# Kernel tuning notes

Hardware: AMD Instinct MI355X
Metric: run time of the kernel (lower is better)

Reference implementation:

```python
import jax, jax.numpy as jnp
import numpy as np

NUM_USERS = 100000
NUM_ITEMS = 50000
NUM_EDGES = 1000000
HIDDEN = 128


def setup_inputs() -> dict:
    key = jax.random.key(0)
    ks = jax.random.split(key, 8)
    z_user = jax.random.normal(ks[0], (NUM_USERS, HIDDEN), dtype=jnp.float32)
    z_item = jax.random.normal(ks[1], (NUM_ITEMS, HIDDEN), dtype=jnp.float32)
    row_idx = jax.random.randint(ks[2], (NUM_EDGES,), 0, NUM_USERS, dtype=jnp.int64 if jax.config.jax_enable_x64 else jnp.int32)
    col_idx = jax.random.randint(ks[3], (NUM_EDGES,), 0, NUM_ITEMS, dtype=jnp.int64 if jax.config.jax_enable_x64 else jnp.int32)
    # Linear params (PyTorch Linear: y = x @ W.T + b); store as [in, out] for einsum.
    scale1 = 1.0 / np.sqrt(2 * HIDDEN)
    scale2 = 1.0 / np.sqrt(HIDDEN)
    W1 = jax.random.uniform(ks[4], (2 * HIDDEN, HIDDEN), jnp.float32, -scale1, scale1)
    b1 = jax.random.uniform(ks[5], (HIDDEN,), jnp.float32, -scale1, scale1)
    W2 = jax.random.uniform(ks[6], (HIDDEN, 1), jnp.float32, -scale2, scale2)
    b2 = jax.random.uniform(ks[7], (1,), jnp.float32, -scale2, scale2)
    return {"z_user": z_user, "z_item": z_item, "row_idx": row_idx,
            "col_idx": col_idx, "W1": W1, "b1": b1, "W2": W2, "b2": b2}


def reference(z_user, z_item, row_idx, col_idx, W1, b1, W2, b2):
    # Gather endpoint embeddings for each candidate edge: [E, H] each.
    zu = z_user[row_idx]
    zi = z_item[col_idx]
    # Equivalent to concat([zu, zi]) @ W1 without materializing the concat:
    h = zu @ W1[:HIDDEN] + zi @ W1[HIDDEN:] + b1  # [E, H]
    h = jax.nn.relu(h)
    out = h @ W2 + b2  # [E, 1]
    return out
```

## Files before the change

kernel.cpp:

```cpp
#include <hip/hip_runtime.h>
#include <hip/hip_bf16.h>
#include <stdint.h>

#define H 128
#define NU 100000
#define NI 50000

typedef __attribute__((ext_vector_type(8))) short short8;
typedef __attribute__((ext_vector_type(4))) float f32x4;

__device__ __forceinline__ uint16_t f2bf(float f) {
    uint32_t x = __float_as_uint(f);
    return (uint16_t)((x + 0x7fffu + ((x >> 16) & 1u)) >> 16);
}
__device__ __forceinline__ uint32_t cvtpk(float lo, float hi) {
    uint32_t r;
    asm("v_cvt_pk_bf16_f32 %0, %1, %2" : "=v"(r) : "v"(lo), "v"(hi));
    return r;
}
__device__ __forceinline__ float cvt_ub0(uint32_t v) { float f; asm("v_cvt_f32_ubyte0 %0, %1" : "=v"(f) : "v"(v)); return f; }
__device__ __forceinline__ float cvt_ub1(uint32_t v) { float f; asm("v_cvt_f32_ubyte1 %0, %1" : "=v"(f) : "v"(v)); return f; }
__device__ __forceinline__ float cvt_ub2(uint32_t v) { float f; asm("v_cvt_f32_ubyte2 %0, %1" : "=v"(f) : "v"(v)); return f; }
__device__ __forceinline__ float cvt_ub3(uint32_t v) { float f; asm("v_cvt_f32_ubyte3 %0, %1" : "=v"(f) : "v"(v)); return f; }

__device__ __forceinline__ int lds_off(int row, int k) {
    return (row * 256 + k * 2) ^ ((row & 7) << 4);
}


__global__ __launch_bounds__(256) void wconv_kernel(
    const float* __restrict__ W1, uint16_t* __restrict__ Wt)
{
    __shared__ char lds[32768];
    const int half = blockIdx.x;
    const float* W = W1 + (size_t)half * H * H;
    uint16_t* Out = Wt + (size_t)half * H * H;
    const int tid = threadIdx.x;

    int n4 = (tid & 31) * 4;
    int k  = tid >> 5;
    #pragma unroll
    for (int p = 0; p < 16; ++p, k += 8) {
        f32x4 v = *(const f32x4*)(W + (size_t)k * H + n4);
        *(uint16_t*)(lds + lds_off(n4 + 0, k)) = f2bf(v.x);
        *(uint16_t*)(lds + lds_off(n4 + 1, k)) = f2bf(v.y);
        *(uint16_t*)(lds + lds_off(n4 + 2, k)) = f2bf(v.z);
        *(uint16_t*)(lds + lds_off(n4 + 3, k)) = f2bf(v.w);
    }
    __syncthreads();
    int n = tid >> 1;
    #pragma unroll
    for (int p = 0; p < 8; ++p) {
        int chunk = (tid & 1) * 8 + p;
        uint4 v = *(const uint4*)(lds + lds_off(n, chunk * 8));
        *(uint4*)(Out + (size_t)n * H + chunk * 8) = v;
    }
}

__global__ __launch_bounds__(256) void proj_kernel(
    const float* __restrict__ z_user, const float* __restrict__ z_item,
    const uint16_t* __restrict__ Wt, const float* __restrict__ b1,
    uint8_t* __restrict__ U8, uint8_t* __restrict__ I8,
    float* __restrict__ Us, float* __restrict__ Is, int nub)
{
    __shared__ char lds[32768];

    int bid = blockIdx.x;
    const float* Z; const uint16_t* Wth; uint8_t* Out8; float* Sc; int M; bool addb1;
    if (bid < nub) { Z = z_user; Wth = Wt;         Out8 = U8; Sc = Us; M = NU; addb1 = false; }
    else { bid -= nub; Z = z_item; Wth = Wt + H*H; Out8 = I8; Sc = Is; M = NI; addb1 = true; }
    const int row0 = bid * 128;
    const int tid = threadIdx.x;

    {
        int n = tid >> 1;
        #pragma unroll
        for (int p = 0; p < 8; ++p) {
            int chunk = (tid & 1) * 8 + p;
            uint4 v = *(const uint4*)(Wth + (size_t)n * H + chunk * 8);
            *(uint4*)(lds + lds_off(n, chunk * 8)) = v;
        }
    }
    __syncthreads();

    const int w  = tid >> 6;
    const int l  = tid & 63;
    const int lr = l & 15;
    const int lk = (l >> 4) * 8;

    int r0 = row0 + w * 32 + lr;
    int r1 = r0 + 16;
    const float* a0p = Z + (size_t)(r0 < M ? r0 : M - 1) * H;
    const float* a1p = Z + (size_t)(r1 < M ? r1 : M - 1) * H;

    f32x4 acc[2][8];
    #pragma unroll
    for (int m0 = 0; m0 < 2; ++m0)
        #pragma unroll
        for (int n0 = 0; n0 < 8; ++n0)
            acc[m0][n0] = (f32x4){0.f, 0.f, 0.f, 0.f};

    #pragma unroll
    for (int kk = 0; kk < 4; ++kk) {
        int kb = kk * 32 + lk;
        f32x4 v00 = *(const f32x4*)(a0p + kb);
        f32x4 v01 = *(const f32x4*)(a0p + kb + 4);
        f32x4 v10 = *(const f32x4*)(a1p + kb);
        f32x4 v11 = *(const f32x4*)(a1p + kb + 4);
        short8 a0, a1;
        uint32_t* A0 = (uint32_t*)&a0;
        uint32_t* A1 = (uint32_t*)&a1;
        A0[0] = cvtpk(v00.x, v00.y); A0[1] = cvtpk(v00.z, v00.w);
        A0[2] = cvtpk(v01.x, v01.y); A0[3] = cvtpk(v01.z, v01.w);
        A1[0] = cvtpk(v10.x, v10.y); A1[1] = cvtpk(v10.z, v10.w);
        A1[2] = cvtpk(v11.x, v11.y); A1[3] = cvtpk(v11.z, v11.w);
        #pragma unroll
        for (int n0 = 0; n0 < 8; ++n0) {
            short8 b = *(const short8*)(lds + lds_off(n0*16 + lr, kb));
            acc[0][n0] = __builtin_amdgcn_mfma_f32_16x16x32_bf16(a0, b, acc[0][n0], 0, 0, 0);
            acc[1][n0] = __builtin_amdgcn_mfma_f32_16x16x32_bf16(a1, b, acc[1][n0], 0, 0, 0);
        }
    }

    float b1v[8];
    #pragma unroll
    for (int n0 = 0; n0 < 8; ++n0) b1v[n0] = addb1 ? b1[n0*16 + lr] : 0.f;

    const int rbase = row0 + w * 32;
    #pragma unroll
    for (int m0 = 0; m0 < 2; ++m0) {
        #pragma unroll
        for (int ri = 0; ri < 4; ++ri) {
            int gr = rbase + m0*16 + (l >> 4) * 4 + ri;
            float v[8];
            float am = 0.f;
            #pragma unroll
            for (int n0 = 0; n0 < 8; ++n0) {
                v[n0] = acc[m0][n0][ri] + b1v[n0];
                am = fmaxf(am, fabsf(v[n0]));
            }
            am = fmaxf(am, __shfl_xor(am, 1));
            am = fmaxf(am, __shfl_xor(am, 2));
            am = fmaxf(am, __shfl_xor(am, 4));
            am = fmaxf(am, __shfl_xor(am, 8));
            float s = am * (1.0f / 127.0f);
            float r = 127.0f / fmaxf(am, 1e-30f);
            uint32_t lo = 0, hi = 0;
            #pragma unroll
            for (int n0 = 0; n0 < 4; ++n0) {
                uint32_t q8 = (uint32_t)fmaf(v[n0], r, 128.5f);
                lo |= q8 << (8 * n0);
            }
            #pragma unroll
            for (int n0 = 4; n0 < 8; ++n0) {
                uint32_t q8 = (uint32_t)fmaf(v[n0], r, 128.5f);
                hi |= q8 << (8 * (n0 - 4));
            }
            if (gr < M) {
                *(uint2*)(Out8 + (size_t)gr * H + lr * 8) = make_uint2(lo, hi);
                if (lr == 0) Sc[gr] = s;
            }
        }
    }
}

__device__ __forceinline__ float edge_dot16(uint4 u, uint4 i, float su, float si,
                                            const float* w2v) {
    const float k = -128.0f * (su + si);
    const uint32_t* up = &u.x;
    const uint32_t* ip = &i.x;
    float acc = 0.f, h;
    #pragma unroll
    for (int d = 0; d < 4; ++d) {
        h = fmaf(su, cvt_ub0(up[d]), fmaf(si, cvt_ub0(ip[d]), k)); acc = fmaf(fmaxf(h, 0.f), w2v[4*d+0], acc);
        h = fmaf(su, cvt_ub1(up[d]), fmaf(si, cvt_ub1(ip[d]), k)); acc = fmaf(fmaxf(h, 0.f), w2v[4*d+1], acc);
        h = fmaf(su, cvt_ub2(up[d]), fmaf(si, cvt_ub2(ip[d]), k)); acc = fmaf(fmaxf(h, 0.f), w2v[4*d+2], acc);
        h = fmaf(su, cvt_ub3(up[d]), fmaf(si, cvt_ub3(ip[d]), k)); acc = fmaf(fmaxf(h, 0.f), w2v[4*d+3], acc);
    }
    return acc;
}

__device__ __forceinline__ float group_reduce8(float acc) {
    acc += __shfl_xor(acc, 4);
    acc += __shfl_xor(acc, 2);
    acc += __shfl_xor(acc, 1);
    return acc;
}

__global__ __launch_bounds__(256) void edge_kernel(
    const uint8_t* __restrict__ U8, const uint8_t* __restrict__ I8,
    const float* __restrict__ Us, const float* __restrict__ Is,
    const int* __restrict__ row_idx, const int* __restrict__ col_idx,
    const float* __restrict__ W2, const float* __restrict__ b2p,
    float* __restrict__ out, int E)
{
    const int l = threadIdx.x & 63;
    const int g = l >> 3;
    const int t = l & 7;

    float w2v[16];
    #pragma unroll
    for (int j = 0; j < 16; ++j) w2v[j] = W2[(j & 7) * 16 + 2 * t + (j >> 3)];
    const float b2 = *b2p;

    const int wid = (int)((blockIdx.x * blockDim.x + threadIdx.x) >> 6);
    const int nw  = (int)((gridDim.x * blockDim.x) >> 6);
    const int stride = nw * 32;
    const int toff = t * 16;

    for (int e0 = wid * 32 + g * 4; e0 + 3 < E; e0 += stride) {
        int4 rp = *(const int4*)(row_idx + e0);
        int4 cp = *(const int4*)(col_idx + e0);
        uint4 u0 = *(const uint4*)(U8 + (uint32_t)(rp.x * H + toff));
        uint4 i0 = *(const uint4*)(I8 + (uint32_t)(cp.x * H + toff));
        uint4 u1 = *(const uint4*)(U8 + (uint32_t)(rp.y * H + toff));
        uint4 i1 = *(const uint4*)(I8 + (uint32_t)(cp.y * H + toff));
        uint4 u2 = *(const uint4*)(U8 + (uint32_t)(rp.z * H + toff));
        uint4 i2 = *(const uint4*)(I8 + (uint32_t)(cp.z * H + toff));
        uint4 u3 = *(const uint4*)(U8 + (uint32_t)(rp.w * H + toff));
        uint4 i3 = *(const uint4*)(I8 + (uint32_t)(cp.w * H + toff));
        float su0 = Us[rp.x], si0 = Is[cp.x];
        float su1 = Us[rp.y], si1 = Is[cp.y];
        float su2 = Us[rp.z], si2 = Is[cp.z];
        float su3 = Us[rp.w], si3 = Is[cp.w];
        float a0 = group_reduce8(edge_dot16(u0, i0, su0, si0, w2v));
        float a1 = group_reduce8(edge_dot16(u1, i1, su1, si1, w2v));
        float a2 = group_reduce8(edge_dot16(u2, i2, su2, si2, w2v));
        float a3 = group_reduce8(edge_dot16(u3, i3, su3, si3, w2v));
        if (t == 0) {
            f32x4 o; o.x = a0 + b2; o.y = a1 + b2; o.z = a2 + b2; o.w = a3 + b2;
            *(f32x4*)(out + e0) = o;
        }
    }
    if (wid == 0 && g == 0) {
        for (int e = (E & ~3); e < E; ++e) {
            int r = row_idx[e], c = col_idx[e];
            uint4 uv = *(const uint4*)(U8 + (uint32_t)(r * H + toff));
            uint4 iv = *(const uint4*)(I8 + (uint32_t)(c * H + toff));
            float acc = group_reduce8(edge_dot16(uv, iv, Us[r], Is[c], w2v));
            if (t == 0) out[e] = acc + b2;
        }
    }
}

extern "C" void kernel_launch(void* const* d_in, const int* in_sizes, int n_in,
                              void* d_out, int out_size, void* d_ws, size_t ws_size,
                              hipStream_t stream) {
    const float* z_user = (const float*)d_in[0];
    const float* z_item = (const float*)d_in[1];
    const int*   row_idx = (const int*)d_in[2];
    const int*   col_idx = (const int*)d_in[3];
    const float* W1 = (const float*)d_in[4];
    const float* b1 = (const float*)d_in[5];
    const float* W2 = (const float*)d_in[6];
    const float* b2 = (const float*)d_in[7];
    float* out = (float*)d_out;
    const int E = in_sizes[2];

    uint8_t* U8 = (uint8_t*)d_ws;
    uint8_t* I8 = U8 + (size_t)NU * H;
    float*   Us = (float*)(I8 + (size_t)NI * H);
    float*   Is = Us + NU;
    uint16_t* Wt = (uint16_t*)(Is + NI);

    const int nub = (NU + 127) / 128;
    const int nib = (NI + 127) / 128;
    wconv_kernel<<<2, 256, 0, stream>>>(W1, Wt);
    proj_kernel<<<nub + nib, 256, 0, stream>>>(z_user, z_item, Wt, b1, U8, I8, Us, Is, nub);
    edge_kernel<<<2048, 256, 0, stream>>>(U8, I8, Us, Is, row_idx, col_idx, W2, b2, out, E);
}
```

Measured before the change: 69.80 us.

## Use 512-thread projection blocks with one M-tile per wave and prefetch edge indices

The projection kernel moves from 256 to 512 threads per block, with each wave handling 16 rows instead of 32. This halves per-thread accumulator registers and doubles waves per block, aiming for better latency hiding on the fp32 embedding loads. The edge kernel now loads the next iteration's row and column indices before gathering the current embeddings, so index-load latency overlaps the dependent gathers. The cost is more waves sharing each LDS copy of the weights, plus extra live registers for the prefetched indices.

```diff
diff --git a/kernel.cpp b/kernel.cpp
--- a/kernel.cpp
+++ b/kernel.cpp
@@ -57,7 +57,7 @@
     }
 }
 
-__global__ __launch_bounds__(256) void proj_kernel(
+__global__ __launch_bounds__(512) void proj_kernel(
     const float* __restrict__ z_user, const float* __restrict__ z_item,
     const uint16_t* __restrict__ Wt, const float* __restrict__ b1,
     uint8_t* __restrict__ U8, uint8_t* __restrict__ I8,
@@ -73,10 +73,10 @@
     const int tid = threadIdx.x;
 
     {
-        int n = tid >> 1;
-        #pragma unroll
-        for (int p = 0; p < 8; ++p) {
-            int chunk = (tid & 1) * 8 + p;
+        int n = tid >> 2;
+        #pragma unroll
+        for (int p = 0; p < 4; ++p) {
+            int chunk = (tid & 3) * 4 + p;
             uint4 v = *(const uint4*)(Wth + (size_t)n * H + chunk * 8);
             *(uint4*)(lds + lds_off(n, chunk * 8)) = v;
         }
@@ -88,37 +88,27 @@
     const int lr = l & 15;
     const int lk = (l >> 4) * 8;
 
-    int r0 = row0 + w * 32 + lr;
-    int r1 = r0 + 16;
+    int r0 = row0 + w * 16 + lr;
     const float* a0p = Z + (size_t)(r0 < M ? r0 : M - 1) * H;
-    const float* a1p = Z + (size_t)(r1 < M ? r1 : M - 1) * H;
-
-    f32x4 acc[2][8];
-    #pragma unroll
-    for (int m0 = 0; m0 < 2; ++m0)
-        #pragma unroll
-        for (int n0 = 0; n0 < 8; ++n0)
-            acc[m0][n0] = (f32x4){0.f, 0.f, 0.f, 0.f};
+
+    f32x4 acc[8];
+    #pragma unroll
+    for (int n0 = 0; n0 < 8; ++n0)
+        acc[n0] = (f32x4){0.f, 0.f, 0.f, 0.f};
 
     #pragma unroll
     for (int kk = 0; kk < 4; ++kk) {
         int kb = kk * 32 + lk;
         f32x4 v00 = *(const f32x4*)(a0p + kb);
         f32x4 v01 = *(const f32x4*)(a0p + kb + 4);
-        f32x4 v10 = *(const f32x4*)(a1p + kb);
-        f32x4 v11 = *(const f32x4*)(a1p + kb + 4);
-        short8 a0, a1;
+        short8 a0;
         uint32_t* A0 = (uint32_t*)&a0;
-        uint32_t* A1 = (uint32_t*)&a1;
         A0[0] = cvtpk(v00.x, v00.y); A0[1] = cvtpk(v00.z, v00.w);
         A0[2] = cvtpk(v01.x, v01.y); A0[3] = cvtpk(v01.z, v01.w);
-        A1[0] = cvtpk(v10.x, v10.y); A1[1] = cvtpk(v10.z, v10.w);
-        A1[2] = cvtpk(v11.x, v11.y); A1[3] = cvtpk(v11.z, v11.w);
         #pragma unroll
         for (int n0 = 0; n0 < 8; ++n0) {
             short8 b = *(const short8*)(lds + lds_off(n0*16 + lr, kb));
-            acc[0][n0] = __builtin_amdgcn_mfma_f32_16x16x32_bf16(a0, b, acc[0][n0], 0, 0, 0);
-            acc[1][n0] = __builtin_amdgcn_mfma_f32_16x16x32_bf16(a1, b, acc[1][n0], 0, 0, 0);
+            acc[n0] = __builtin_amdgcn_mfma_f32_16x16x32_bf16(a0, b, acc[n0], 0, 0, 0);
         }
     }
 
@@ -126,40 +116,37 @@
     #pragma unroll
     for (int n0 = 0; n0 < 8; ++n0) b1v[n0] = addb1 ? b1[n0*16 + lr] : 0.f;
 
-    const int rbase = row0 + w * 32;
-    #pragma unroll
-    for (int m0 = 0; m0 < 2; ++m0) {
-        #pragma unroll
-        for (int ri = 0; ri < 4; ++ri) {
-            int gr = rbase + m0*16 + (l >> 4) * 4 + ri;
-            float v[8];
-            float am = 0.f;
-            #pragma unroll
-            for (int n0 = 0; n0 < 8; ++n0) {
-                v[n0] = acc[m0][n0][ri] + b1v[n0];
-                am = fmaxf(am, fabsf(v[n0]));
-            }
-            am = fmaxf(am, __shfl_xor(am, 1));
-            am = fmaxf(am, __shfl_xor(am, 2));
-            am = fmaxf(am, __shfl_xor(am, 4));
-            am = fmaxf(am, __shfl_xor(am, 8));
-            float s = am * (1.0f / 127.0f);
-            float r = 127.0f / fmaxf(am, 1e-30f);
-            uint32_t lo = 0, hi = 0;
-            #pragma unroll
-            for (int n0 = 0; n0 < 4; ++n0) {
-                uint32_t q8 = (uint32_t)fmaf(v[n0], r, 128.5f);
-                lo |= q8 << (8 * n0);
-            }
-            #pragma unroll
-            for (int n0 = 4; n0 < 8; ++n0) {
-                uint32_t q8 = (uint32_t)fmaf(v[n0], r, 128.5f);
-                hi |= q8 << (8 * (n0 - 4));
-            }
-            if (gr < M) {
-                *(uint2*)(Out8 + (size_t)gr * H + lr * 8) = make_uint2(lo, hi);
-                if (lr == 0) Sc[gr] = s;
-            }
+    const int rbase = row0 + w * 16;
+    #pragma unroll
+    for (int ri = 0; ri < 4; ++ri) {
+        int gr = rbase + (l >> 4) * 4 + ri;
+        float v[8];
+        float am = 0.f;
+        #pragma unroll
+        for (int n0 = 0; n0 < 8; ++n0) {
+            v[n0] = acc[n0][ri] + b1v[n0];
+            am = fmaxf(am, fabsf(v[n0]));
+        }
+        am = fmaxf(am, __shfl_xor(am, 1));
+        am = fmaxf(am, __shfl_xor(am, 2));
+        am = fmaxf(am, __shfl_xor(am, 4));
+        am = fmaxf(am, __shfl_xor(am, 8));
+        float s = am * (1.0f / 127.0f);
+        float r = 127.0f / fmaxf(am, 1e-30f);
+        uint32_t lo = 0, hi = 0;
+        #pragma unroll
+        for (int n0 = 0; n0 < 4; ++n0) {
+            uint32_t q8 = (uint32_t)fmaf(v[n0], r, 128.5f);
+            lo |= q8 << (8 * n0);
+        }
+        #pragma unroll
+        for (int n0 = 4; n0 < 8; ++n0) {
+            uint32_t q8 = (uint32_t)fmaf(v[n0], r, 128.5f);
+            hi |= q8 << (8 * (n0 - 4));
+        }
+        if (gr < M) {
+            *(uint2*)(Out8 + (size_t)gr * H + lr * 8) = make_uint2(lo, hi);
+            if (lr == 0) Sc[gr] = s;
         }
     }
 }
@@ -207,29 +194,39 @@
     const int nw  = (int)((gridDim.x * blockDim.x) >> 6);
     const int stride = nw * 32;
     const int toff = t * 16;
-
-    for (int e0 = wid * 32 + g * 4; e0 + 3 < E; e0 += stride) {
+    const int e0 = wid * 32 + g * 4;
+
+    if (e0 + 3 < E) {
         int4 rp = *(const int4*)(row_idx + e0);
         int4 cp = *(const int4*)(col_idx + e0);
-        uint4 u0 = *(const uint4*)(U8 + (uint32_t)(rp.x * H + toff));
-        uint4 i0 = *(const uint4*)(I8 + (uint32_t)(cp.x * H + toff));
-        uint4 u1 = *(const uint4*)(U8 + (uint32_t)(rp.y * H + toff));
-        uint4 i1 = *(const uint4*)(I8 + (uint32_t)(cp.y * H + toff));
-        uint4 u2 = *(const uint4*)(U8 + (uint32_t)(rp.z * H + toff));
-        uint4 i2 = *(const uint4*)(I8 + (uint32_t)(cp.z * H + toff));
-        uint4 u3 = *(const uint4*)(U8 + (uint32_t)(rp.w * H + toff));
-        uint4 i3 = *(const uint4*)(I8 + (uint32_t)(cp.w * H + toff));
-        float su0 = Us[rp.x], si0 = Is[cp.x];
-        float su1 = Us[rp.y], si1 = Is[cp.y];
-        float su2 = Us[rp.z], si2 = Is[cp.z];
-        float su3 = Us[rp.w], si3 = Is[cp.w];
-        float a0 = group_reduce8(edge_dot16(u0, i0, su0, si0, w2v));
-        float a1 = group_reduce8(edge_dot16(u1, i1, su1, si1, w2v));
-        float a2 = group_reduce8(edge_dot16(u2, i2, su2, si2, w2v));
-        float a3 = group_reduce8(edge_dot16(u3, i3, su3, si3, w2v));
-        if (t == 0) {
-            f32x4 o; o.x = a0 + b2; o.y = a1 + b2; o.z = a2 + b2; o.w = a3 + b2;
-            *(f32x4*)(out + e0) = o;
+        for (int e = e0; e + 3 < E; e += stride) {
+            int en = e + stride;
+            int4 rpn = rp, cpn = cp;
+            if (en + 3 < E) {
+                rpn = *(const int4*)(row_idx + en);
+                cpn = *(const int4*)(col_idx + en);
+            }
+            uint4 u0 = *(const uint4*)(U8 + (uint32_t)(rp.x * H + toff));
+            uint4 i0 = *(const uint4*)(I8 + (uint32_t)(cp.x * H + toff));
+            uint4 u1 = *(const uint4*)(U8 + (uint32_t)(rp.y * H + toff));
+            uint4 i1 = *(const uint4*)(I8 + (uint32_t)(cp.y * H + toff));
+            uint4 u2 = *(const uint4*)(U8 + (uint32_t)(rp.z * H + toff));
+            uint4 i2 = *(const uint4*)(I8 + (uint32_t)(cp.z * H + toff));
+            uint4 u3 = *(const uint4*)(U8 + (uint32_t)(rp.w * H + toff));
+            uint4 i3 = *(const uint4*)(I8 + (uint32_t)(cp.w * H + toff));
+            float su0 = Us[rp.x], si0 = Is[cp.x];
+            float su1 = Us[rp.y], si1 = Is[cp.y];
+            float su2 = Us[rp.z], si2 = Is[cp.z];
+            float su3 = Us[rp.w], si3 = Is[cp.w];
+            float a0 = group_reduce8(edge_dot16(u0, i0, su0, si0, w2v));
+            float a1 = group_reduce8(edge_dot16(u1, i1, su1, si1, w2v));
+            float a2 = group_reduce8(edge_dot16(u2, i2, su2, si2, w2v));
+            float a3 = group_reduce8(edge_dot16(u3, i3, su3, si3, w2v));
+            if (t == 0) {
+                f32x4 o; o.x = a0 + b2; o.y = a1 + b2; o.z = a2 + b2; o.w = a3 + b2;
+                *(f32x4*)(out + e) = o;
+            }
+            rp = rpn; cp = cpn;
         }
     }
     if (wid == 0 && g == 0) {
@@ -266,6 +263,6 @@
     const int nub = (NU + 127) / 128;
     const int nib = (NI + 127) / 128;
     wconv_kernel<<<2, 256, 0, stream>>>(W1, Wt);
-    proj_kernel<<<nub + nib, 256, 0, stream>>>(z_user, z_item, Wt, b1, U8, I8, Us, Is, nub);
+    proj_kernel<<<nub + nib, 512, 0, stream>>>(z_user, z_item, Wt, b1, U8, I8, Us, Is, nub);
     edge_kernel<<<2048, 256, 0, stream>>>(U8, I8, Us, Is, row_idx, col_idx, W2, b2, out, E);
 }
```

Result: faster. 64.23 us (-8.0%).
